# Performance work log

Hardware: AMD Instinct MI355X
Metric: run time of the kernel (lower is better)

## Reference

```python
import jax, jax.numpy as jnp
import numpy as np

B, T, IN, H, OUT = 256, 512, 128, 1024, 9  # batch, seq_len, input_size, hidden_dim, output_size(=9 coords)


def setup_inputs() -> dict:
    key = jax.random.key(0)
    ks = jax.random.split(key, 10)
    rn = lambda k, sh: jax.random.normal(k, sh, dtype=jnp.float32) * 0.05
    return {
        "x": rn(ks[0], (B, T, IN)),
        "W_ih": rn(ks[1], (4 * H, IN + OUT)),   # LSTMCell input weights (input_size + 9)
        "b_ih": rn(ks[2], (4 * H,)),
        "W_hh": rn(ks[3], (4 * H, H)),
        "b_hh": rn(ks[4], (4 * H,)),
        "W_h2h": rn(ks[5], (H, H)),
        "b_h2h": rn(ks[6], (H,)),
        "W_h2o": rn(ks[7], (OUT, H)),
        "b_h2o": rn(ks[8], (OUT,)),
        "lengths": jax.random.randint(ks[9], (B,), 1, T + 1).astype(jnp.int32),
    }


def reference(x, W_ih, b_ih, W_hh, b_hh, W_h2h, b_h2h, W_h2o, b_h2o, lengths):
    # Faithful to SimpleCharRNN.forward with use_corrector_flag=False (default):
    # per timestep: concat(x_t, prev_output) -> LSTMCell -> h2h -> h2o,
    # and NOTE the h2h output replaces h as the recurrent hidden state.
    batch = x.shape[0]
    hid = W_hh.shape[1]
    out_dim = W_h2o.shape[0]

    def step(carry, xt):
        h, c, out_prev = carry
        inp = jnp.concatenate([xt, out_prev], axis=-1)           # [B, IN+9]
        gates = inp @ W_ih.T + b_ih + h @ W_hh.T + b_hh          # [B, 4H]
        i, f, g, o = jnp.split(gates, 4, axis=-1)                # torch LSTMCell gate order
        i = jax.nn.sigmoid(i)
        f = jax.nn.sigmoid(f)
        g = jnp.tanh(g)
        o = jax.nn.sigmoid(o)
        c_new = f * c + i * g
        h_cell = o * jnp.tanh(c_new)
        h_new = h_cell @ W_h2h.T + b_h2h                         # h <- h2h(h)
        out_new = h_new @ W_h2o.T + b_h2o                        # output_i = h2o(h)
        return (h_new, c_new, out_new), out_new

    h0 = jnp.zeros((batch, hid), x.dtype)
    c0 = jnp.zeros((batch, hid), x.dtype)
    o0 = jnp.zeros((batch, out_dim), x.dtype)
    _, outs = jax.lax.scan(step, (h0, c0, o0), jnp.swapaxes(x, 0, 1))  # outs: [T, B, 9]
    answer = jnp.swapaxes(outs, 0, 1)                            # [B, T, 9]
    return answer, lengths
```

## Files before the change

kernel.cpp:

```cpp
#include <hip/hip_runtime.h>
#include <math.h>

#define TB 256
#define TT 512
#define TIN 128
#define TH 1024
#define TOUT 9
#define KD 1152

typedef _Float16 half8 __attribute__((ext_vector_type(8)));
typedef float f32x4 __attribute__((ext_vector_type(4)));

#define OB_WHF   0ull
#define SB_WHF   (128ull*2*36*64*8*2)
#define OB_WCB   (OB_WHF + SB_WHF)
#define SB_WCB   (9ull*1024*4)
#define OB_BCB   (OB_WCB + SB_WCB)
#define SB_BCB   64ull
#define OB_B0    (OB_BCB + SB_BCB)
#define SB_B0    (4096ull*4)
#define OB_BC    (OB_B0 + SB_B0)
#define SB_BC    (4096ull*4)
#define OB_H0    (OB_BC + SB_BC)
#define SB_H     (256ull*1024*2)
#define OB_H1    (OB_H0 + SB_H)
#define OB_GC    (OB_H1 + SB_H)
#define OB_END   (OB_GC + 8192ull)

__device__ __forceinline__ size_t frag_addr(int col, int k) {
  int q = col >> 10, hcol = col & 1023;
  int wcg = hcol >> 3, jj = hcol & 7;
  int c = (q << 3) | jj;
  int nt = c >> 4, n = c & 15;
  int kc = k >> 5, ls = (k >> 3) & 3, je = k & 7;
  return ((((size_t)wcg * 2 + nt) * 36 + kc) * 64 + ((ls << 4) | n)) * 8 + je;
}

__device__ __forceinline__ void st_h2_agent(_Float16* p, _Float16 v) {
  union { _Float16 h; unsigned short u; } c; c.h = v;
  __hip_atomic_store((unsigned short*)p, c.u, __ATOMIC_RELAXED, __HIP_MEMORY_SCOPE_AGENT);
}


__global__ __launch_bounds__(256) void k_combo(const float* __restrict__ W_h2o,
                                               const float* __restrict__ W_h2h,
                                               const float* __restrict__ b_h2h,
                                               const float* __restrict__ b_h2o,
                                               float* __restrict__ Wcombo,
                                               float* __restrict__ bcombo) {
  int gid = blockIdx.x * 256 + threadIdx.x;
  if (gid < 9 * 1024) {
    int r = gid >> 10, m = gid & 1023;
    float s = 0.f;
    for (int j = 0; j < 1024; ++j) s += W_h2o[r * 1024 + j] * W_h2h[j * 1024 + m];
    Wcombo[gid] = s;
  }
  if (gid < 9) {
    float s = b_h2o[gid];
    for (int j = 0; j < 1024; ++j) s += W_h2o[gid * 1024 + j] * b_h2h[j];
    bcombo[gid] = s;
  }
}

__global__ __launch_bounds__(256) void k_wblk(const float* __restrict__ W_hh,
                                              const float* __restrict__ W_ih,
                                              const float* __restrict__ W_h2o,
                                              const float* __restrict__ W_h2h,
                                              _Float16* __restrict__ Whf) {
  __shared__ float As2[16][68];
  __shared__ float Bs[16][68];
  __shared__ float Wio_s[64][12];
  __shared__ float Bo[9][16];
  const int tid = threadIdx.x;
  const int bm = (blockIdx.x & 15) * 64;
  const int bc = (blockIdx.x >> 4) * 64;
  const int tx = tid & 15, ty = tid >> 4;
  const int cl = tid >> 2, kq4 = tid & 3;

  for (int i = tid; i < 64 * 9; i += 256) {
    int row = i / 9, r = i % 9;
    Wio_s[row][r] = W_ih[(size_t)(bc + row) * 137 + 128 + r];
  }

  float acc[4][4];
#pragma unroll
  for (int i = 0; i < 4; ++i)
#pragma unroll
    for (int j = 0; j < 4; ++j) acc[i][j] = 0.f;

  for (int k0 = 0; k0 < 1024; k0 += 16) {
    __syncthreads();
    if (tid < 144) { int r = tid >> 4, kk = tid & 15; Bo[r][kk] = W_h2o[(size_t)r * 1024 + k0 + kk]; }
    { int kk = tid >> 4, q = tid & 15;
      float4 v = *(const float4*)(W_h2h + (size_t)(k0 + kk) * 1024 + bm + q * 4);
      *(float4*)&Bs[kk][q * 4] = v; }
    float4 av = *(const float4*)(W_hh + (size_t)(bc + cl) * 1024 + k0 + kq4 * 4);
    __syncthreads();
    {
      float c0 = 0.f, c1 = 0.f, c2 = 0.f, c3 = 0.f;
#pragma unroll
      for (int r = 0; r < 9; ++r) {
        float wio = Wio_s[cl][r];
        c0 += wio * Bo[r][kq4 * 4 + 0];
        c1 += wio * Bo[r][kq4 * 4 + 1];
        c2 += wio * Bo[r][kq4 * 4 + 2];
        c3 += wio * Bo[r][kq4 * 4 + 3];
      }
      As2[kq4 * 4 + 0][cl] = av.x + c0;
      As2[kq4 * 4 + 1][cl] = av.y + c1;
      As2[kq4 * 4 + 2][cl] = av.z + c2;
      As2[kq4 * 4 + 3][cl] = av.w + c3;
    }
    __syncthreads();
#pragma unroll
    for (int kk = 0; kk < 16; ++kk) {
      float4 a = *(const float4*)&As2[kk][ty * 4];
      float4 bv = *(const float4*)&Bs[kk][tx * 4];
      acc[0][0] += a.x * bv.x; acc[0][1] += a.x * bv.y; acc[0][2] += a.x * bv.z; acc[0][3] += a.x * bv.w;
      acc[1][0] += a.y * bv.x; acc[1][1] += a.y * bv.y; acc[1][2] += a.y * bv.z; acc[1][3] += a.y * bv.w;
      acc[2][0] += a.z * bv.x; acc[2][1] += a.z * bv.y; acc[2][2] += a.z * bv.z; acc[2][3] += a.z * bv.w;
      acc[3][0] += a.w * bv.x; acc[3][1] += a.w * bv.y; acc[3][2] += a.w * bv.z; acc[3][3] += a.w * bv.w;
    }
  }
#pragma unroll
  for (int i = 0; i < 4; ++i)
#pragma unroll
    for (int j = 0; j < 4; ++j) {
      int col = bc + ty * 4 + i;
      int m = bm + tx * 4 + j;
      Whf[frag_addr(col, 128 + m)] = (_Float16)acc[i][j];
    }
}

__global__ __launch_bounds__(256) void k_bias(const float* __restrict__ b_ih,
                                              const float* __restrict__ b_hh,
                                              const float* __restrict__ W_hh,
                                              const float* __restrict__ W_ih,
                                              const float* __restrict__ b_h2h,
                                              const float* __restrict__ bcombo,
                                              float* __restrict__ b0,
                                              float* __restrict__ bconst) {
  int col = blockIdx.x * 256 + threadIdx.x;
  float base = b_ih[col] + b_hh[col];
  b0[col] = base;
  float s = 0.f;
  for (int j = 0; j < 1024; ++j) s += W_hh[(size_t)col * 1024 + j] * b_h2h[j];
#pragma unroll
  for (int r = 0; r < 9; ++r) s += W_ih[(size_t)col * 137 + 128 + r] * bcombo[r];
  bconst[col] = base + s;
}

__global__ __launch_bounds__(256) void k_fillx(const float* __restrict__ W_ih,
                                               _Float16* __restrict__ Whf) {
  int gid = blockIdx.x * 256 + threadIdx.x;
  int col = gid >> 7, k = gid & 127;
  Whf[frag_addr(col, k)] = (_Float16)W_ih[(size_t)col * 137 + k];
}

__global__ void k_len(const int* __restrict__ len, float* __restrict__ dout) {
  int i = threadIdx.x;
  if (i < TB) dout[(size_t)TB * TT * TOUT + i] = (float)len[i];
}


__device__ __forceinline__ float sigm(float v) { return 1.f / (1.f + __expf(-v)); }
__device__ __forceinline__ float tanh_f(float v) {
  float e2 = __expf(2.f * v);
  return (e2 - 1.f) / (e2 + 1.f);
}

#define KEEP14(a) asm volatile("" :: "v"(a[0]), "v"(a[1]), "v"(a[2]), "v"(a[3]), \
  "v"(a[4]), "v"(a[5]), "v"(a[6]), "v"(a[7]), "v"(a[8]), "v"(a[9]), "v"(a[10]), \
  "v"(a[11]), "v"(a[12]), "v"(a[13]))
#define KEEP18(a) asm volatile("" :: "v"(a[0]), "v"(a[1]), "v"(a[2]), "v"(a[3]), \
  "v"(a[4]), "v"(a[5]), "v"(a[6]), "v"(a[7]), "v"(a[8]), "v"(a[9]), "v"(a[10]), \
  "v"(a[11]), "v"(a[12]), "v"(a[13]), "v"(a[14]), "v"(a[15]), "v"(a[16]), "v"(a[17]))

__global__ __launch_bounds__(512, 2) void k_main(const float* __restrict__ x,
                                                 const _Float16* __restrict__ Whf,
                                                 const float* __restrict__ Wc,
                                                 const float* __restrict__ b0,
                                                 const float* __restrict__ bcf,
                                                 const float* __restrict__ bcombo,
                                                 _Float16* __restrict__ hA,
                                                 _Float16* __restrict__ hB,
                                                 unsigned* __restrict__ gs,
                                                 float* __restrict__ dout) {
  __shared__ _Float16 Wl[2 * 36 * 64 * 8];
  __shared__ float gbuf[2][128][36];
  __shared__ float Wc_s[9][1024];
  __shared__ float bias_s[2][32];
  __shared__ float bco_s[12];
  __shared__ int sAbort;

  const int bx = blockIdx.x;
  const int half_id = bx >> 7;
  const int wcg = bx & 127;
  const int B0 = half_id * 128;
  const int myb = B0 + wcg;
  const int grp = wcg >> 4;
  const int tid = threadIdx.x;
  const int lane = tid & 63;
  const int wv = tid >> 6;
  const int mp = wv & 3, kh = wv >> 2;

  const size_t CH = (size_t)TB * 8;

  unsigned* hbase = gs + half_id * 1024;
  unsigned* gcnt_grp = hbase + grp * 32;
  unsigned* gcnt_root = hbase + 8 * 32;
  unsigned* gabort = gs + 1984;

  {
    const uint4* src = (const uint4*)(Whf + (size_t)wcg * (2 * 36 * 64 * 8));
    uint4* dst = (uint4*)Wl;
    for (int i = tid; i < 2 * 36 * 64 * 8 / 8; i += 512) dst[i] = src[i];
  }
  {
    const float4* src = (const float4*)Wc;
    float4* dst = (float4*)&Wc_s[0][0];
    for (int i = tid; i < 9 * 1024 / 4; i += 512) dst[i] = src[i];
  }
  if (tid == 0) sAbort = 0;
  if (tid < 9) bco_s[tid] = bcombo[tid];
  if (tid < 32) {
    int g = (tid >> 3) * 1024 + wcg * 8 + (tid & 7);
    bias_s[0][tid] = b0[g];
    bias_s[1][tid] = bcf[g];
  }
  float cs0 = 0.f, cs1 = 0.f;
  __syncthreads();

  const _Float16* ha = hA;
  _Float16* hn = hB;

  const int bA0 = B0 + mp * 32 + (lane & 15);
  const int bA1 = bA0 + 16;
  const int ko = (lane >> 4) * 8;
  const int chb = lane >> 4;
  const _Float16* wlb = Wl + (size_t)lane * 8 + (size_t)(kh * 18) * 512;
  unsigned myLead = 0;

  f32x4 acc00 = {0.f, 0.f, 0.f, 0.f};
  f32x4 acc01 = {0.f, 0.f, 0.f, 0.f};
  f32x4 acc10 = {0.f, 0.f, 0.f, 0.f};
  f32x4 acc11 = {0.f, 0.f, 0.f, 0.f};

#define XPART(tt) do { \
    const float* x0_ = x + ((size_t)bA0 * TT + (tt)) * TIN; \
    const float* x1_ = x + ((size_t)bA1 * TT + (tt)) * TIN; \
    _Pragma("unroll") \
    for (int i_ = 0; i_ < 4; ++i_) { \
      float4 p0 = *(const float4*)(x0_ + i_ * 32 + ko); \
      float4 p1 = *(const float4*)(x0_ + i_ * 32 + ko + 4); \
      float4 q0 = *(const float4*)(x1_ + i_ * 32 + ko); \
      float4 q1 = *(const float4*)(x1_ + i_ * 32 + ko + 4); \
      half8 v0_, v1_; \
      v0_[0] = (_Float16)p0.x; v0_[1] = (_Float16)p0.y; v0_[2] = (_Float16)p0.z; v0_[3] = (_Float16)p0.w; \
      v0_[4] = (_Float16)p1.x; v0_[5] = (_Float16)p1.y; v0_[6] = (_Float16)p1.z; v0_[7] = (_Float16)p1.w; \
      v1_[0] = (_Float16)q0.x; v1_[1] = (_Float16)q0.y; v1_[2] = (_Float16)q0.z; v1_[3] = (_Float16)q0.w; \
      v1_[4] = (_Float16)q1.x; v1_[5] = (_Float16)q1.y; v1_[6] = (_Float16)q1.z; v1_[7] = (_Float16)q1.w; \
      half8 bf0_ = *(const half8*)(wlb + (size_t)i_ * 512); \
      half8 bf1_ = *(const half8*)(wlb + (size_t)(36 + i_) * 512); \
      acc00 = __builtin_amdgcn_mfma_f32_16x16x32_f16(v0_, bf0_, acc00, 0, 0, 0); \
      acc01 = __builtin_amdgcn_mfma_f32_16x16x32_f16(v0_, bf1_, acc01, 0, 0, 0); \
      acc10 = __builtin_amdgcn_mfma_f32_16x16x32_f16(v1_, bf0_, acc10, 0, 0, 0); \
      acc11 = __builtin_amdgcn_mfma_f32_16x16x32_f16(v1_, bf1_, acc11, 0, 0, 0); \
    } \
  } while (0)

  if (kh == 0) XPART(0);

  for (int t = 0; t < TT; ++t) {
    const _Float16* hb0 = ha + (size_t)chb * CH + (size_t)bA0 * 8;
    const _Float16* hb1 = ha + (size_t)chb * CH + (size_t)bA1 * 8;
    if (kh == 0) {
      half8 a0[14], a1[14];
#pragma unroll
      for (int i = 0; i < 14; ++i) {
        a0[i] = *(const half8*)(hb0 + (size_t)(4 * (4 + i) - 16) * CH);
        a1[i] = *(const half8*)(hb1 + (size_t)(4 * (4 + i) - 16) * CH);
      }
      KEEP14(a0); KEEP14(a1);
      __builtin_amdgcn_sched_barrier(0);
#pragma unroll
      for (int i = 0; i < 14; ++i) {
        const int lc = 4 + i;
        half8 bf0 = *(const half8*)(wlb + (size_t)lc * 512);
        half8 bf1 = *(const half8*)(wlb + (size_t)(36 + lc) * 512);
        acc00 = __builtin_amdgcn_mfma_f32_16x16x32_f16(a0[i], bf0, acc00, 0, 0, 0);
        acc01 = __builtin_amdgcn_mfma_f32_16x16x32_f16(a0[i], bf1, acc01, 0, 0, 0);
        acc10 = __builtin_amdgcn_mfma_f32_16x16x32_f16(a1[i], bf0, acc10, 0, 0, 0);
        acc11 = __builtin_amdgcn_mfma_f32_16x16x32_f16(a1[i], bf1, acc11, 0, 0, 0);
      }
    } else {
      half8 a0[18], a1[18];
#pragma unroll
      for (int i = 0; i < 18; ++i) {
        a0[i] = *(const half8*)(hb0 + (size_t)(4 * i + 56) * CH);
        a1[i] = *(const half8*)(hb1 + (size_t)(4 * i + 56) * CH);
      }
      KEEP18(a0); KEEP18(a1);
      __builtin_amdgcn_sched_barrier(0);
#pragma unroll
      for (int i = 0; i < 18; ++i) {
        half8 bf0 = *(const half8*)(wlb + (size_t)i * 512);
        half8 bf1 = *(const half8*)(wlb + (size_t)(36 + i) * 512);
        acc00 = __builtin_amdgcn_mfma_f32_16x16x32_f16(a0[i], bf0, acc00, 0, 0, 0);
        acc01 = __builtin_amdgcn_mfma_f32_16x16x32_f16(a0[i], bf1, acc01, 0, 0, 0);
        acc10 = __builtin_amdgcn_mfma_f32_16x16x32_f16(a1[i], bf0, acc10, 0, 0, 0);
        acc11 = __builtin_amdgcn_mfma_f32_16x16x32_f16(a1[i], bf1, acc11, 0, 0, 0);
      }
    }
    {
      int rb0 = mp * 32 + (lane >> 4) * 4;
      int rb1 = rb0 + 16;
      int cc = lane & 15;
#pragma unroll
      for (int r = 0; r < 4; ++r) {
        gbuf[kh][rb0 + r][cc] = acc00[r];
        gbuf[kh][rb0 + r][16 + cc] = acc01[r];
        gbuf[kh][rb1 + r][cc] = acc10[r];
        gbuf[kh][rb1 + r][16 + cc] = acc11[r];
      }
    }
    __syncthreads();

    {
      const int fb = tid >> 3, fj = tid & 7;
      const float* bs = bias_s[(t > 0) ? 1 : 0];
      float vi = gbuf[0][fb][fj]      + gbuf[1][fb][fj]      + bs[fj];
      float vf = gbuf[0][fb][8 + fj]  + gbuf[1][fb][8 + fj]  + bs[8 + fj];
      float vg = gbuf[0][fb][16 + fj] + gbuf[1][fb][16 + fj] + bs[16 + fj];
      float vo = gbuf[0][fb][24 + fj] + gbuf[1][fb][24 + fj] + bs[24 + fj];
      float ig = sigm(vi), fg = sigm(vf), gg = tanh_f(vg), og = sigm(vo);
      float cn = fg * cs0 + ig * gg;
      cs0 = cn;
      st_h2_agent(hn + (size_t)wcg * CH + (size_t)(B0 + fb) * 8 + fj,
                  (_Float16)(og * tanh_f(cn)));

      const int fb2 = fb + 64;
      float vi2 = gbuf[0][fb2][fj]      + gbuf[1][fb2][fj]      + bs[fj];
      float vf2 = gbuf[0][fb2][8 + fj]  + gbuf[1][fb2][8 + fj]  + bs[8 + fj];
      float vg2 = gbuf[0][fb2][16 + fj] + gbuf[1][fb2][16 + fj] + bs[16 + fj];
      float vo2 = gbuf[0][fb2][24 + fj] + gbuf[1][fb2][24 + fj] + bs[24 + fj];
      float ig2 = sigm(vi2), fg2 = sigm(vf2), gg2 = tanh_f(vg2), og2 = sigm(vo2);
      float cn2 = fg2 * cs1 + ig2 * gg2;
      cs1 = cn2;
      st_h2_agent(hn + (size_t)wcg * CH + (size_t)(B0 + fb2) * 8 + fj,
                  (_Float16)(og2 * tanh_f(cn2)));
    }
    __threadfence_block();
    __syncthreads();

    if (tid == 0) {
      unsigned old = __hip_atomic_fetch_add(gcnt_grp, 1u, __ATOMIC_RELAXED, __HIP_MEMORY_SCOPE_AGENT);
      myLead = (old == (unsigned)(t + 1) * 16u - 1u);
      if (myLead)
        __hip_atomic_fetch_add(gcnt_root, 1u, __ATOMIC_RELAXED, __HIP_MEMORY_SCOPE_AGENT);
    }

    if (t > 0) {
      const _Float16* hxb = ha + (size_t)myb * 8;
      {
        float s = 0.f;
#pragma unroll
        for (int p = 0; p < 2; ++p) {
          int ch = 2 * lane + p;
          half8 hv = *(const half8*)(hxb + (size_t)ch * CH);
          const float* wr = &Wc_s[wv][ch * 8];
#pragma unroll
          for (int j = 0; j < 8; ++j) s += (float)hv[j] * wr[j];
        }
#pragma unroll
        for (int off = 32; off > 0; off >>= 1) s += __shfl_down(s, off, 64);
        if (lane == 0) dout[((size_t)myb * TT + (t - 1)) * TOUT + wv] = s + bco_s[wv];
      }
      if (wv == 0) {
        const float* wr8 = &Wc_s[8][0];
        float s = 0.f;
#pragma unroll
        for (int p = 0; p < 2; ++p) {
          int ch = 2 * lane + p;
          half8 hv = *(const half8*)(hxb + (size_t)ch * CH);
#pragma unroll
          for (int j = 0; j < 8; ++j) s += (float)hv[j] * wr8[ch * 8 + j];
        }
#pragma unroll
        for (int off = 32; off > 0; off >>= 1) s += __shfl_down(s, off, 64);
        if (lane == 0) dout[((size_t)myb * TT + (t - 1)) * TOUT + 8] = s + bco_s[8];
      }
    }

    acc00 = (f32x4){0.f, 0.f, 0.f, 0.f};
    acc01 = (f32x4){0.f, 0.f, 0.f, 0.f};
    acc10 = (f32x4){0.f, 0.f, 0.f, 0.f};
    acc11 = (f32x4){0.f, 0.f, 0.f, 0.f};
    if (kh == 0 && t + 1 < TT) XPART(t + 1);

    if (tid == 0) {
      bool ab = false;
      unsigned guard = 0;
      const unsigned tgt = (unsigned)(t + 1) * 8u;
      while (__hip_atomic_load(gcnt_root, __ATOMIC_RELAXED, __HIP_MEMORY_SCOPE_AGENT) < tgt) {
        __builtin_amdgcn_s_sleep(1);
        if (((++guard) & 255u) == 0u &&
            __hip_atomic_load(gabort, __ATOMIC_RELAXED, __HIP_MEMORY_SCOPE_AGENT) != 0u) { ab = true; break; }
        if (guard > 200000u) {
          __hip_atomic_store(gabort, 1u, __ATOMIC_RELAXED, __HIP_MEMORY_SCOPE_AGENT);
          ab = true; break;
        }
      }
      if (ab) {
        sAbort = 1;
      } else {
        (void)__hip_atomic_load(gcnt_root, __ATOMIC_ACQUIRE, __HIP_MEMORY_SCOPE_AGENT);
      }
    }
    __syncthreads();
    if (sAbort) return;

    const _Float16* tp = ha; ha = hn; hn = (_Float16*)tp;
  }

  {
    const _Float16* hxb = ha + (size_t)myb * 8;
    {
      float s = 0.f;
#pragma unroll
      for (int p = 0; p < 2; ++p) {
        int ch = 2 * lane + p;
        half8 hv = *(const half8*)(hxb + (size_t)ch * CH);
        const float* wr = &Wc_s[wv][ch * 8];
#pragma unroll
        for (int j = 0; j < 8; ++j) s += (float)hv[j] * wr[j];
      }
#pragma unroll
      for (int off = 32; off > 0; off >>= 1) s += __shfl_down(s, off, 64);
      if (lane == 0) dout[((size_t)myb * TT + (TT - 1)) * TOUT + wv] = s + bco_s[wv];
    }
    if (wv == 0) {
      const float* wr8 = &Wc_s[8][0];
      float s = 0.f;
#pragma unroll
      for (int p = 0; p < 2; ++p) {
        int ch = 2 * lane + p;
        half8 hv = *(const half8*)(hxb + (size_t)ch * CH);
#pragma unroll
        for (int j = 0; j < 8; ++j) s += (float)hv[j] * wr8[ch * 8 + j];
      }
#pragma unroll
      for (int off = 32; off > 0; off >>= 1) s += __shfl_down(s, off, 64);
      if (lane == 0) dout[((size_t)myb * TT + (TT - 1)) * TOUT + 8] = s + bco_s[8];
    }
  }
}


extern "C" void kernel_launch(void* const* d_in, const int* in_sizes, int n_in,
                              void* d_out, int out_size, void* d_ws, size_t ws_size,
                              hipStream_t stream) {
  if (ws_size < OB_END) return;

  const float* x     = (const float*)d_in[0];
  const float* W_ih  = (const float*)d_in[1];
  const float* b_ih  = (const float*)d_in[2];
  const float* W_hh  = (const float*)d_in[3];
  const float* b_hh  = (const float*)d_in[4];
  const float* W_h2h = (const float*)d_in[5];
  const float* b_h2h = (const float*)d_in[6];
  const float* W_h2o = (const float*)d_in[7];
  const float* b_h2o = (const float*)d_in[8];
  const int*   lens  = (const int*)d_in[9];

  char* ws = (char*)d_ws;
  float* dout    = (float*)d_out;
  _Float16* Whf  = (_Float16*)(ws + OB_WHF);
  float* Wcombo  = (float*)(ws + OB_WCB);
  float* bcombo  = (float*)(ws + OB_BCB);
  float* b0      = (float*)(ws + OB_B0);
  float* bconst  = (float*)(ws + OB_BC);
  _Float16* h0   = (_Float16*)(ws + OB_H0);
  _Float16* h1   = (_Float16*)(ws + OB_H1);
  unsigned* gs   = (unsigned*)(ws + OB_GC);

  hipMemsetAsync((void*)(ws + OB_H0), 0, OB_END - OB_H0, stream);

  k_combo<<<36, 256, 0, stream>>>(W_h2o, W_h2h, b_h2h, b_h2o, Wcombo, bcombo);
  k_wblk<<<1024, 256, 0, stream>>>(W_hh, W_ih, W_h2o, W_h2h, Whf);
  k_bias<<<16, 256, 0, stream>>>(b_ih, b_hh, W_hh, W_ih, b_h2h, bcombo, b0, bconst);
  k_fillx<<<2048, 256, 0, stream>>>(W_ih, Whf);
  k_len<<<1, 256, 0, stream>>>(lens, dout);

  k_main<<<256, 512, 0, stream>>>(x, Whf, Wcombo, b0, bconst, bcombo, h0, h1, gs, dout);
}
```

Measured before the change: 5.049 ms.

## Double block size to 1024 threads and split K reduction across four wave groups

```diff
diff --git a/kernel.cpp b/kernel.cpp
--- a/kernel.cpp
+++ b/kernel.cpp
@@ -169,25 +169,22 @@
   return (e2 - 1.f) / (e2 + 1.f);
 }
 
-#define KEEP14(a) asm volatile("" :: "v"(a[0]), "v"(a[1]), "v"(a[2]), "v"(a[3]), \
-  "v"(a[4]), "v"(a[5]), "v"(a[6]), "v"(a[7]), "v"(a[8]), "v"(a[9]), "v"(a[10]), \
-  "v"(a[11]), "v"(a[12]), "v"(a[13]))
-#define KEEP18(a) asm volatile("" :: "v"(a[0]), "v"(a[1]), "v"(a[2]), "v"(a[3]), \
-  "v"(a[4]), "v"(a[5]), "v"(a[6]), "v"(a[7]), "v"(a[8]), "v"(a[9]), "v"(a[10]), \
-  "v"(a[11]), "v"(a[12]), "v"(a[13]), "v"(a[14]), "v"(a[15]), "v"(a[16]), "v"(a[17]))
-
-__global__ __launch_bounds__(512, 2) void k_main(const float* __restrict__ x,
-                                                 const _Float16* __restrict__ Whf,
-                                                 const float* __restrict__ Wc,
-                                                 const float* __restrict__ b0,
-                                                 const float* __restrict__ bcf,
-                                                 const float* __restrict__ bcombo,
-                                                 _Float16* __restrict__ hA,
-                                                 _Float16* __restrict__ hB,
-                                                 unsigned* __restrict__ gs,
-                                                 float* __restrict__ dout) {
+#define KEEP5(a) asm volatile("" :: "v"(a[0]), "v"(a[1]), "v"(a[2]), "v"(a[3]), "v"(a[4]))
+#define KEEP9(a) asm volatile("" :: "v"(a[0]), "v"(a[1]), "v"(a[2]), "v"(a[3]), \
+  "v"(a[4]), "v"(a[5]), "v"(a[6]), "v"(a[7]), "v"(a[8]))
+
+__global__ __launch_bounds__(1024, 4) void k_main(const float* __restrict__ x,
+                                                  const _Float16* __restrict__ Whf,
+                                                  const float* __restrict__ Wc,
+                                                  const float* __restrict__ b0,
+                                                  const float* __restrict__ bcf,
+                                                  const float* __restrict__ bcombo,
+                                                  _Float16* __restrict__ hA,
+                                                  _Float16* __restrict__ hB,
+                                                  unsigned* __restrict__ gs,
+                                                  float* __restrict__ dout) {
   __shared__ _Float16 Wl[2 * 36 * 64 * 8];
-  __shared__ float gbuf[2][128][36];
+  __shared__ _Float16 gbuf[4][128][36];
   __shared__ float Wc_s[9][1024];
   __shared__ float bias_s[2][32];
   __shared__ float bco_s[12];
@@ -202,7 +199,7 @@
   const int tid = threadIdx.x;
   const int lane = tid & 63;
   const int wv = tid >> 6;
-  const int mp = wv & 3, kh = wv >> 2;
+  const int mp = wv & 3, kq = wv >> 2;
 
   const size_t CH = (size_t)TB * 8;
 
@@ -214,12 +211,12 @@
   {
     const uint4* src = (const uint4*)(Whf + (size_t)wcg * (2 * 36 * 64 * 8));
     uint4* dst = (uint4*)Wl;
-    for (int i = tid; i < 2 * 36 * 64 * 8 / 8; i += 512) dst[i] = src[i];
+    for (int i = tid; i < 2 * 36 * 64 * 8 / 8; i += 1024) dst[i] = src[i];
   }
   {
     const float4* src = (const float4*)Wc;
     float4* dst = (float4*)&Wc_s[0][0];
-    for (int i = tid; i < 9 * 1024 / 4; i += 512) dst[i] = src[i];
+    for (int i = tid; i < 9 * 1024 / 4; i += 1024) dst[i] = src[i];
   }
   if (tid == 0) sAbort = 0;
   if (tid < 9) bco_s[tid] = bcombo[tid];
@@ -228,7 +225,7 @@
     bias_s[0][tid] = b0[g];
     bias_s[1][tid] = bcf[g];
   }
-  float cs0 = 0.f, cs1 = 0.f;
+  float cs = 0.f;
   __syncthreads();
 
   const _Float16* ha = hA;
@@ -238,7 +235,7 @@
   const int bA1 = bA0 + 16;
   const int ko = (lane >> 4) * 8;
   const int chb = lane >> 4;
-  const _Float16* wlb = Wl + (size_t)lane * 8 + (size_t)(kh * 18) * 512;
+  const _Float16* wlb = Wl + (size_t)lane * 8;
   unsigned myLead = 0;
 
   f32x4 acc00 = {0.f, 0.f, 0.f, 0.f};
@@ -269,43 +266,44 @@
     } \
   } while (0)
 
-  if (kh == 0) XPART(0);
+  if (kq == 0) XPART(0);
 
   for (int t = 0; t < TT; ++t) {
     const _Float16* hb0 = ha + (size_t)chb * CH + (size_t)bA0 * 8;
     const _Float16* hb1 = ha + (size_t)chb * CH + (size_t)bA1 * 8;
-    if (kh == 0) {
-      half8 a0[14], a1[14];
-#pragma unroll
-      for (int i = 0; i < 14; ++i) {
-        a0[i] = *(const half8*)(hb0 + (size_t)(4 * (4 + i) - 16) * CH);
-        a1[i] = *(const half8*)(hb1 + (size_t)(4 * (4 + i) - 16) * CH);
-      }
-      KEEP14(a0); KEEP14(a1);
+    if (kq == 0) {
+      half8 a0[5], a1[5];
+#pragma unroll
+      for (int i = 0; i < 5; ++i) {
+        a0[i] = *(const half8*)(hb0 + (size_t)(4 * i) * CH);
+        a1[i] = *(const half8*)(hb1 + (size_t)(4 * i) * CH);
+      }
+      KEEP5(a0); KEEP5(a1);
       __builtin_amdgcn_sched_barrier(0);
 #pragma unroll
-      for (int i = 0; i < 14; ++i) {
-        const int lc = 4 + i;
-        half8 bf0 = *(const half8*)(wlb + (size_t)lc * 512);
-        half8 bf1 = *(const half8*)(wlb + (size_t)(36 + lc) * 512);
+      for (int i = 0; i < 5; ++i) {
+        const int kcg = 4 + i;
+        half8 bf0 = *(const half8*)(wlb + (size_t)kcg * 512);
+        half8 bf1 = *(const half8*)(wlb + (size_t)(36 + kcg) * 512);
         acc00 = __builtin_amdgcn_mfma_f32_16x16x32_f16(a0[i], bf0, acc00, 0, 0, 0);
         acc01 = __builtin_amdgcn_mfma_f32_16x16x32_f16(a0[i], bf1, acc01, 0, 0, 0);
         acc10 = __builtin_amdgcn_mfma_f32_16x16x32_f16(a1[i], bf0, acc10, 0, 0, 0);
         acc11 = __builtin_amdgcn_mfma_f32_16x16x32_f16(a1[i], bf1, acc11, 0, 0, 0);
       }
     } else {
-      half8 a0[18], a1[18];
-#pragma unroll
-      for (int i = 0; i < 18; ++i) {
-        a0[i] = *(const half8*)(hb0 + (size_t)(4 * i + 56) * CH);
-        a1[i] = *(const half8*)(hb1 + (size_t)(4 * i + 56) * CH);
-      }
-      KEEP18(a0); KEEP18(a1);
+      half8 a0[9], a1[9];
+#pragma unroll
+      for (int i = 0; i < 9; ++i) {
+        a0[i] = *(const half8*)(hb0 + (size_t)(4 * (9 * kq + i) - 16) * CH);
+        a1[i] = *(const half8*)(hb1 + (size_t)(4 * (9 * kq + i) - 16) * CH);
+      }
+      KEEP9(a0); KEEP9(a1);
       __builtin_amdgcn_sched_barrier(0);
 #pragma unroll
-      for (int i = 0; i < 18; ++i) {
-        half8 bf0 = *(const half8*)(wlb + (size_t)i * 512);
-        half8 bf1 = *(const half8*)(wlb + (size_t)(36 + i) * 512);
+      for (int i = 0; i < 9; ++i) {
+        const int kcg = 9 * kq + i;
+        half8 bf0 = *(const half8*)(wlb + (size_t)kcg * 512);
+        half8 bf1 = *(const half8*)(wlb + (size_t)(36 + kcg) * 512);
         acc00 = __builtin_amdgcn_mfma_f32_16x16x32_f16(a0[i], bf0, acc00, 0, 0, 0);
         acc01 = __builtin_amdgcn_mfma_f32_16x16x32_f16(a0[i], bf1, acc01, 0, 0, 0);
         acc10 = __builtin_amdgcn_mfma_f32_16x16x32_f16(a1[i], bf0, acc10, 0, 0, 0);
@@ -318,10 +316,10 @@
       int cc = lane & 15;
 #pragma unroll
       for (int r = 0; r < 4; ++r) {
-        gbuf[kh][rb0 + r][cc] = acc00[r];
-        gbuf[kh][rb0 + r][16 + cc] = acc01[r];
-        gbuf[kh][rb1 + r][cc] = acc10[r];
-        gbuf[kh][rb1 + r][16 + cc] = acc11[r];
+        gbuf[kq][rb0 + r][cc] = (_Float16)acc00[r];
+        gbuf[kq][rb0 + r][16 + cc] = (_Float16)acc01[r];
+        gbuf[kq][rb1 + r][cc] = (_Float16)acc10[r];
+        gbuf[kq][rb1 + r][16 + cc] = (_Float16)acc11[r];
       }
     }
     __syncthreads();
@@ -329,26 +327,19 @@
     {
       const int fb = tid >> 3, fj = tid & 7;
       const float* bs = bias_s[(t > 0) ? 1 : 0];
-      float vi = gbuf[0][fb][fj]      + gbuf[1][fb][fj]      + bs[fj];
-      float vf = gbuf[0][fb][8 + fj]  + gbuf[1][fb][8 + fj]  + bs[8 + fj];
-      float vg = gbuf[0][fb][16 + fj] + gbuf[1][fb][16 + fj] + bs[16 + fj];
-      float vo = gbuf[0][fb][24 + fj] + gbuf[1][fb][24 + fj] + bs[24 + fj];
+      float vi = (float)gbuf[0][fb][fj]      + (float)gbuf[1][fb][fj]
+               + (float)gbuf[2][fb][fj]      + (float)gbuf[3][fb][fj]      + bs[fj];
+      float vf = (float)gbuf[0][fb][8 + fj]  + (float)gbuf[1][fb][8 + fj]
+               + (float)gbuf[2][fb][8 + fj]  + (float)gbuf[3][fb][8 + fj]  + bs[8 + fj];
+      float vg = (float)gbuf[0][fb][16 + fj] + (float)gbuf[1][fb][16 + fj]
+               + (float)gbuf[2][fb][16 + fj] + (float)gbuf[3][fb][16 + fj] + bs[16 + fj];
+      float vo = (float)gbuf[0][fb][24 + fj] + (float)gbuf[1][fb][24 + fj]
+               + (float)gbuf[2][fb][24 + fj] + (float)gbuf[3][fb][24 + fj] + bs[24 + fj];
       float ig = sigm(vi), fg = sigm(vf), gg = tanh_f(vg), og = sigm(vo);
-      float cn = fg * cs0 + ig * gg;
-      cs0 = cn;
+      float cn = fg * cs + ig * gg;
+      cs = cn;
       st_h2_agent(hn + (size_t)wcg * CH + (size_t)(B0 + fb) * 8 + fj,
                   (_Float16)(og * tanh_f(cn)));
-
-      const int fb2 = fb + 64;
-      float vi2 = gbuf[0][fb2][fj]      + gbuf[1][fb2][fj]      + bs[fj];
-      float vf2 = gbuf[0][fb2][8 + fj]  + gbuf[1][fb2][8 + fj]  + bs[8 + fj];
-      float vg2 = gbuf[0][fb2][16 + fj] + gbuf[1][fb2][16 + fj] + bs[16 + fj];
-      float vo2 = gbuf[0][fb2][24 + fj] + gbuf[1][fb2][24 + fj] + bs[24 + fj];
-      float ig2 = sigm(vi2), fg2 = sigm(vf2), gg2 = tanh_f(vg2), og2 = sigm(vo2);
-      float cn2 = fg2 * cs1 + ig2 * gg2;
-      cs1 = cn2;
-      st_h2_agent(hn + (size_t)wcg * CH + (size_t)(B0 + fb2) * 8 + fj,
-                  (_Float16)(og2 * tanh_f(cn2)));
     }
     __threadfence_block();
     __syncthreads();
@@ -360,43 +351,27 @@
         __hip_atomic_fetch_add(gcnt_root, 1u, __ATOMIC_RELAXED, __HIP_MEMORY_SCOPE_AGENT);
     }
 
-    if (t > 0) {
+    if (t > 0 && wv < 9) {
       const _Float16* hxb = ha + (size_t)myb * 8;
-      {
-        float s = 0.f;
-#pragma unroll
-        for (int p = 0; p < 2; ++p) {
-          int ch = 2 * lane + p;
-          half8 hv = *(const half8*)(hxb + (size_t)ch * CH);
-          const float* wr = &Wc_s[wv][ch * 8];
-#pragma unroll
-          for (int j = 0; j < 8; ++j) s += (float)hv[j] * wr[j];
-        }
-#pragma unroll
-        for (int off = 32; off > 0; off >>= 1) s += __shfl_down(s, off, 64);
-        if (lane == 0) dout[((size_t)myb * TT + (t - 1)) * TOUT + wv] = s + bco_s[wv];
-      }
-      if (wv == 0) {
-        const float* wr8 = &Wc_s[8][0];
-        float s = 0.f;
-#pragma unroll
-        for (int p = 0; p < 2; ++p) {
-          int ch = 2 * lane + p;
-          half8 hv = *(const half8*)(hxb + (size_t)ch * CH);
-#pragma unroll
-          for (int j = 0; j < 8; ++j) s += (float)hv[j] * wr8[ch * 8 + j];
-        }
-#pragma unroll
-        for (int off = 32; off > 0; off >>= 1) s += __shfl_down(s, off, 64);
-        if (lane == 0) dout[((size_t)myb * TT + (t - 1)) * TOUT + 8] = s + bco_s[8];
-      }
+      float s = 0.f;
+#pragma unroll
+      for (int p = 0; p < 2; ++p) {
+        int ch = 2 * lane + p;
+        half8 hv = *(const half8*)(hxb + (size_t)ch * CH);
+        const float* wr = &Wc_s[wv][ch * 8];
+#pragma unroll
+        for (int j = 0; j < 8; ++j) s += (float)hv[j] * wr[j];
+      }
+#pragma unroll
+      for (int off = 32; off > 0; off >>= 1) s += __shfl_down(s, off, 64);
+      if (lane == 0) dout[((size_t)myb * TT + (t - 1)) * TOUT + wv] = s + bco_s[wv];
     }
 
     acc00 = (f32x4){0.f, 0.f, 0.f, 0.f};
     acc01 = (f32x4){0.f, 0.f, 0.f, 0.f};
     acc10 = (f32x4){0.f, 0.f, 0.f, 0.f};
     acc11 = (f32x4){0.f, 0.f, 0.f, 0.f};
-    if (kh == 0 && t + 1 < TT) XPART(t + 1);
+    if (kq == 0 && t + 1 < TT) XPART(t + 1);
 
     if (tid == 0) {
       bool ab = false;
@@ -423,36 +398,20 @@
     const _Float16* tp = ha; ha = hn; hn = (_Float16*)tp;
   }
 
-  {
+  if (wv < 9) {
     const _Float16* hxb = ha + (size_t)myb * 8;
-    {
-      float s = 0.f;
-#pragma unroll
-      for (int p = 0; p < 2; ++p) {
-        int ch = 2 * lane + p;
-        half8 hv = *(const half8*)(hxb + (size_t)ch * CH);
-        const float* wr = &Wc_s[wv][ch * 8];
-#pragma unroll
-        for (int j = 0; j < 8; ++j) s += (float)hv[j] * wr[j];
-      }
-#pragma unroll
-      for (int off = 32; off > 0; off >>= 1) s += __shfl_down(s, off, 64);
-      if (lane == 0) dout[((size_t)myb * TT + (TT - 1)) * TOUT + wv] = s + bco_s[wv];
-    }
-    if (wv == 0) {
-      const float* wr8 = &Wc_s[8][0];
-      float s = 0.f;
-#pragma unroll
-      for (int p = 0; p < 2; ++p) {
-        int ch = 2 * lane + p;
-        half8 hv = *(const half8*)(hxb + (size_t)ch * CH);
-#pragma unroll
-        for (int j = 0; j < 8; ++j) s += (float)hv[j] * wr8[ch * 8 + j];
-      }
-#pragma unroll
-      for (int off = 32; off > 0; off >>= 1) s += __shfl_down(s, off, 64);
-      if (lane == 0) dout[((size_t)myb * TT + (TT - 1)) * TOUT + 8] = s + bco_s[8];
-    }
+    float s = 0.f;
+#pragma unroll
+    for (int p = 0; p < 2; ++p) {
+      int ch = 2 * lane + p;
+      half8 hv = *(const half8*)(hxb + (size_t)ch * CH);
+      const float* wr = &Wc_s[wv][ch * 8];
+#pragma unroll
+      for (int j = 0; j < 8; ++j) s += (float)hv[j] * wr[j];
+    }
+#pragma unroll
+    for (int off = 32; off > 0; off >>= 1) s += __shfl_down(s, off, 64);
+    if (lane == 0) dout[((size_t)myb * TT + (TT - 1)) * TOUT + wv] = s + bco_s[wv];
   }
 }
 
@@ -492,5 +451,5 @@
   k_fillx<<<2048, 256, 0, stream>>>(W_ih, Whf);
   k_len<<<1, 256, 0, stream>>>(lens, dout);
 
-  k_main<<<256, 512, 0, stream>>>(x, Whf, Wcombo, b0, bconst, bcombo, h0, h1, gs, dout);
-}
+  k_main<<<256, 1024, 0, stream>>>(x, Whf, Wcombo, b0, bconst, bcombo, h0, h1, gs, dout);
+}
```

After: 6.236 ms. +23.5%, slower.

## Retile recurrent LSTM kernel to 64-batch quarters with 16 hidden columns per block

Applied to the files above, without the earlier changes.

```diff
diff --git a/kernel.cpp b/kernel.cpp
--- a/kernel.cpp
+++ b/kernel.cpp
@@ -12,7 +12,7 @@
 typedef float f32x4 __attribute__((ext_vector_type(4)));
 
 #define OB_WHF   0ull
-#define SB_WHF   (128ull*2*36*64*8*2)
+#define SB_WHF   (64ull*4*36*64*8*2)
 #define OB_WCB   (OB_WHF + SB_WHF)
 #define SB_WCB   (9ull*1024*4)
 #define OB_BCB   (OB_WCB + SB_WCB)
@@ -29,11 +29,9 @@
 
 __device__ __forceinline__ size_t frag_addr(int col, int k) {
   int q = col >> 10, hcol = col & 1023;
-  int wcg = hcol >> 3, jj = hcol & 7;
-  int c = (q << 3) | jj;
-  int nt = c >> 4, n = c & 15;
+  int wcg2 = hcol >> 4, jj = hcol & 15;
   int kc = k >> 5, ls = (k >> 3) & 3, je = k & 7;
-  return ((((size_t)wcg * 2 + nt) * 36 + kc) * 64 + ((ls << 4) | n)) * 8 + je;
+  return ((((size_t)wcg2 * 4 + q) * 36 + kc) * 64 + ((ls << 4) | jj)) * 8 + je;
 }
 
 __device__ __forceinline__ void st_h2_agent(_Float16* p, _Float16 v) {
@@ -186,48 +184,45 @@
                                                  _Float16* __restrict__ hB,
                                                  unsigned* __restrict__ gs,
                                                  float* __restrict__ dout) {
-  __shared__ _Float16 Wl[2 * 36 * 64 * 8];
-  __shared__ float gbuf[2][128][36];
-  __shared__ float Wc_s[9][1024];
-  __shared__ float bias_s[2][32];
-  __shared__ float bco_s[12];
+  __shared__ _Float16 Wl[4 * 36 * 64 * 8];
+  __shared__ _Float16 gbuf[64][72];
   __shared__ int sAbort;
 
   const int bx = blockIdx.x;
-  const int half_id = bx >> 7;
-  const int wcg = bx & 127;
-  const int B0 = half_id * 128;
-  const int myb = B0 + wcg;
-  const int grp = wcg >> 4;
+  const int qd = bx >> 6;
+  const int wcg2 = bx & 63;
+  const int B0 = qd * 64;
+  const int myb = B0 + wcg2;
+  const int grp = wcg2 >> 3;
   const int tid = threadIdx.x;
   const int lane = tid & 63;
   const int wv = tid >> 6;
-  const int mp = wv & 3, kh = wv >> 2;
+  const int mp = wv & 1, np = (wv >> 1) & 1, kh = wv >> 2;
 
   const size_t CH = (size_t)TB * 8;
 
-  unsigned* hbase = gs + half_id * 1024;
-  unsigned* gcnt_grp = hbase + grp * 32;
-  unsigned* gcnt_root = hbase + 8 * 32;
-  unsigned* gabort = gs + 1984;
+  unsigned* qbase = gs + qd * 512;
+  unsigned* gcnt_grp = qbase + grp * 32;
+  unsigned* gcnt_root = qbase + 8 * 32;
+  unsigned* gabort = gs + 500;
 
   {
-    const uint4* src = (const uint4*)(Whf + (size_t)wcg * (2 * 36 * 64 * 8));
+    const uint4* src = (const uint4*)(Whf + (size_t)wcg2 * (4 * 36 * 64 * 8));
     uint4* dst = (uint4*)Wl;
-    for (int i = tid; i < 2 * 36 * 64 * 8 / 8; i += 512) dst[i] = src[i];
-  }
-  {
-    const float4* src = (const float4*)Wc;
-    float4* dst = (float4*)&Wc_s[0][0];
-    for (int i = tid; i < 9 * 1024 / 4; i += 512) dst[i] = src[i];
+    for (int i = tid; i < 4 * 36 * 64 * 8 / 8; i += 512) dst[i] = src[i];
   }
   if (tid == 0) sAbort = 0;
-  if (tid < 9) bco_s[tid] = bcombo[tid];
-  if (tid < 32) {
-    int g = (tid >> 3) * 1024 + wcg * 8 + (tid & 7);
-    bias_s[0][tid] = b0[g];
-    bias_s[1][tid] = bcf[g];
-  }
+
+  const int fb_i = tid >> 3, fj_i = tid & 7;
+  const int cb = wcg2 * 16;
+  float bC0 = bcf[cb + fj_i],          bC1 = bcf[1024 + cb + fj_i];
+  float bC2 = bcf[2048 + cb + fj_i],   bC3 = bcf[3072 + cb + fj_i];
+  float bC4 = bcf[cb + 8 + fj_i],      bC5 = bcf[1024 + cb + 8 + fj_i];
+  float bC6 = bcf[2048 + cb + 8 + fj_i], bC7 = bcf[3072 + cb + 8 + fj_i];
+  float bZ0 = b0[cb + fj_i],           bZ1 = b0[1024 + cb + fj_i];
+  float bZ2 = b0[2048 + cb + fj_i],    bZ3 = b0[3072 + cb + fj_i];
+  float bZ4 = b0[cb + 8 + fj_i],       bZ5 = b0[1024 + cb + 8 + fj_i];
+  float bZ6 = b0[2048 + cb + 8 + fj_i], bZ7 = b0[3072 + cb + 8 + fj_i];
   float cs0 = 0.f, cs1 = 0.f;
   __syncthreads();
 
@@ -238,7 +233,8 @@
   const int bA1 = bA0 + 16;
   const int ko = (lane >> 4) * 8;
   const int chb = lane >> 4;
-  const _Float16* wlb = Wl + (size_t)lane * 8 + (size_t)(kh * 18) * 512;
+  const _Float16* wlb0 = Wl + (size_t)(2 * np) * 18432 + (size_t)lane * 8;
+  const _Float16* wlb1 = wlb0 + 18432;
   unsigned myLead = 0;
 
   f32x4 acc00 = {0.f, 0.f, 0.f, 0.f};
@@ -260,8 +256,8 @@
       v0_[4] = (_Float16)p1.x; v0_[5] = (_Float16)p1.y; v0_[6] = (_Float16)p1.z; v0_[7] = (_Float16)p1.w; \
       v1_[0] = (_Float16)q0.x; v1_[1] = (_Float16)q0.y; v1_[2] = (_Float16)q0.z; v1_[3] = (_Float16)q0.w; \
       v1_[4] = (_Float16)q1.x; v1_[5] = (_Float16)q1.y; v1_[6] = (_Float16)q1.z; v1_[7] = (_Float16)q1.w; \
-      half8 bf0_ = *(const half8*)(wlb + (size_t)i_ * 512); \
-      half8 bf1_ = *(const half8*)(wlb + (size_t)(36 + i_) * 512); \
+      half8 bf0_ = *(const half8*)(wlb0 + (size_t)i_ * 512); \
+      half8 bf1_ = *(const half8*)(wlb1 + (size_t)i_ * 512); \
       acc00 = __builtin_amdgcn_mfma_f32_16x16x32_f16(v0_, bf0_, acc00, 0, 0, 0); \
       acc01 = __builtin_amdgcn_mfma_f32_16x16x32_f16(v0_, bf1_, acc01, 0, 0, 0); \
       acc10 = __builtin_amdgcn_mfma_f32_16x16x32_f16(v1_, bf0_, acc10, 0, 0, 0); \
@@ -278,16 +274,16 @@
       half8 a0[14], a1[14];
 #pragma unroll
       for (int i = 0; i < 14; ++i) {
-        a0[i] = *(const half8*)(hb0 + (size_t)(4 * (4 + i) - 16) * CH);
-        a1[i] = *(const half8*)(hb1 + (size_t)(4 * (4 + i) - 16) * CH);
+        a0[i] = *(const half8*)(hb0 + (size_t)(4 * i) * CH);
+        a1[i] = *(const half8*)(hb1 + (size_t)(4 * i) * CH);
       }
       KEEP14(a0); KEEP14(a1);
       __builtin_amdgcn_sched_barrier(0);
 #pragma unroll
       for (int i = 0; i < 14; ++i) {
-        const int lc = 4 + i;
-        half8 bf0 = *(const half8*)(wlb + (size_t)lc * 512);
-        half8 bf1 = *(const half8*)(wlb + (size_t)(36 + lc) * 512);
+        const int kcg = 4 + i;
+        half8 bf0 = *(const half8*)(wlb0 + (size_t)kcg * 512);
+        half8 bf1 = *(const half8*)(wlb1 + (size_t)kcg * 512);
         acc00 = __builtin_amdgcn_mfma_f32_16x16x32_f16(a0[i], bf0, acc00, 0, 0, 0);
         acc01 = __builtin_amdgcn_mfma_f32_16x16x32_f16(a0[i], bf1, acc01, 0, 0, 0);
         acc10 = __builtin_amdgcn_mfma_f32_16x16x32_f16(a1[i], bf0, acc10, 0, 0, 0);
@@ -304,8 +300,9 @@
       __builtin_amdgcn_sched_barrier(0);
 #pragma unroll
       for (int i = 0; i < 18; ++i) {
-        half8 bf0 = *(const half8*)(wlb + (size_t)i * 512);
-        half8 bf1 = *(const half8*)(wlb + (size_t)(36 + i) * 512);
+        const int kcg = 18 + i;
+        half8 bf0 = *(const half8*)(wlb0 + (size_t)kcg * 512);
+        half8 bf1 = *(const half8*)(wlb1 + (size_t)kcg * 512);
         acc00 = __builtin_amdgcn_mfma_f32_16x16x32_f16(a0[i], bf0, acc00, 0, 0, 0);
         acc01 = __builtin_amdgcn_mfma_f32_16x16x32_f16(a0[i], bf1, acc01, 0, 0, 0);
         acc10 = __builtin_amdgcn_mfma_f32_16x16x32_f16(a1[i], bf0, acc10, 0, 0, 0);
@@ -315,39 +312,53 @@
     {
       int rb0 = mp * 32 + (lane >> 4) * 4;
       int rb1 = rb0 + 16;
-      int cc = lane & 15;
-#pragma unroll
-      for (int r = 0; r < 4; ++r) {
-        gbuf[kh][rb0 + r][cc] = acc00[r];
-        gbuf[kh][rb0 + r][16 + cc] = acc01[r];
-        gbuf[kh][rb1 + r][cc] = acc10[r];
-        gbuf[kh][rb1 + r][16 + cc] = acc11[r];
-      }
-    }
-    __syncthreads();
+      int cc0 = np * 32 + (lane & 15);
+      int cc1 = cc0 + 16;
+      if (kh == 0) {
+#pragma unroll
+        for (int r = 0; r < 4; ++r) {
+          gbuf[rb0 + r][cc0] = (_Float16)acc00[r];
+          gbuf[rb0 + r][cc1] = (_Float16)acc01[r];
+          gbuf[rb1 + r][cc0] = (_Float16)acc10[r];
+          gbuf[rb1 + r][cc1] = (_Float16)acc11[r];
+        }
+      }
+      __syncthreads();
+      if (kh == 1) {
+#pragma unroll
+        for (int r = 0; r < 4; ++r) {
+          gbuf[rb0 + r][cc0] = (_Float16)((float)gbuf[rb0 + r][cc0] + acc00[r]);
+          gbuf[rb0 + r][cc1] = (_Float16)((float)gbuf[rb0 + r][cc1] + acc01[r]);
+          gbuf[rb1 + r][cc0] = (_Float16)((float)gbuf[rb1 + r][cc0] + acc10[r]);
+          gbuf[rb1 + r][cc1] = (_Float16)((float)gbuf[rb1 + r][cc1] + acc11[r]);
+        }
+      }
+      __syncthreads();
+    }
 
     {
-      const int fb = tid >> 3, fj = tid & 7;
-      const float* bs = bias_s[(t > 0) ? 1 : 0];
-      float vi = gbuf[0][fb][fj]      + gbuf[1][fb][fj]      + bs[fj];
-      float vf = gbuf[0][fb][8 + fj]  + gbuf[1][fb][8 + fj]  + bs[8 + fj];
-      float vg = gbuf[0][fb][16 + fj] + gbuf[1][fb][16 + fj] + bs[16 + fj];
-      float vo = gbuf[0][fb][24 + fj] + gbuf[1][fb][24 + fj] + bs[24 + fj];
+      const bool later = (t > 0);
+      float b_0 = later ? bC0 : bZ0, b_1 = later ? bC1 : bZ1;
+      float b_2 = later ? bC2 : bZ2, b_3 = later ? bC3 : bZ3;
+      float b_4 = later ? bC4 : bZ4, b_5 = later ? bC5 : bZ5;
+      float b_6 = later ? bC6 : bZ6, b_7 = later ? bC7 : bZ7;
+      float vi = (float)gbuf[fb_i][fj_i]      + b_0;
+      float vf = (float)gbuf[fb_i][16 + fj_i] + b_1;
+      float vg = (float)gbuf[fb_i][32 + fj_i] + b_2;
+      float vo = (float)gbuf[fb_i][48 + fj_i] + b_3;
       float ig = sigm(vi), fg = sigm(vf), gg = tanh_f(vg), og = sigm(vo);
       float cn = fg * cs0 + ig * gg;
       cs0 = cn;
-      st_h2_agent(hn + (size_t)wcg * CH + (size_t)(B0 + fb) * 8 + fj,
+      st_h2_agent(hn + (size_t)(2 * wcg2) * CH + (size_t)(B0 + fb_i) * 8 + fj_i,
                   (_Float16)(og * tanh_f(cn)));
-
-      const int fb2 = fb + 64;
-      float vi2 = gbuf[0][fb2][fj]      + gbuf[1][fb2][fj]      + bs[fj];
-      float vf2 = gbuf[0][fb2][8 + fj]  + gbuf[1][fb2][8 + fj]  + bs[8 + fj];
-      float vg2 = gbuf[0][fb2][16 + fj] + gbuf[1][fb2][16 + fj] + bs[16 + fj];
-      float vo2 = gbuf[0][fb2][24 + fj] + gbuf[1][fb2][24 + fj] + bs[24 + fj];
+      float vi2 = (float)gbuf[fb_i][8 + fj_i]  + b_4;
+      float vf2 = (float)gbuf[fb_i][24 + fj_i] + b_5;
+      float vg2 = (float)gbuf[fb_i][40 + fj_i] + b_6;
+      float vo2 = (float)gbuf[fb_i][56 + fj_i] + b_7;
       float ig2 = sigm(vi2), fg2 = sigm(vf2), gg2 = tanh_f(vg2), og2 = sigm(vo2);
       float cn2 = fg2 * cs1 + ig2 * gg2;
       cs1 = cn2;
-      st_h2_agent(hn + (size_t)wcg * CH + (size_t)(B0 + fb2) * 8 + fj,
+      st_h2_agent(hn + (size_t)(2 * wcg2 + 1) * CH + (size_t)(B0 + fb_i) * 8 + fj_i,
                   (_Float16)(og2 * tanh_f(cn2)));
     }
     __threadfence_block();
@@ -355,7 +366,7 @@
 
     if (tid == 0) {
       unsigned old = __hip_atomic_fetch_add(gcnt_grp, 1u, __ATOMIC_RELAXED, __HIP_MEMORY_SCOPE_AGENT);
-      myLead = (old == (unsigned)(t + 1) * 16u - 1u);
+      myLead = (old == (unsigned)(t + 1) * 8u - 1u);
       if (myLead)
         __hip_atomic_fetch_add(gcnt_root, 1u, __ATOMIC_RELAXED, __HIP_MEMORY_SCOPE_AGENT);
     }
@@ -363,32 +374,36 @@
     if (t > 0) {
       const _Float16* hxb = ha + (size_t)myb * 8;
       {
+        const float* wcp = Wc + (size_t)wv * 1024;
         float s = 0.f;
 #pragma unroll
         for (int p = 0; p < 2; ++p) {
           int ch = 2 * lane + p;
           half8 hv = *(const half8*)(hxb + (size_t)ch * CH);
-          const float* wr = &Wc_s[wv][ch * 8];
-#pragma unroll
-          for (int j = 0; j < 8; ++j) s += (float)hv[j] * wr[j];
+          float4 wa = *(const float4*)(wcp + ch * 8);
+          float4 wb = *(const float4*)(wcp + ch * 8 + 4);
+          s += (float)hv[0] * wa.x + (float)hv[1] * wa.y + (float)hv[2] * wa.z + (float)hv[3] * wa.w
+             + (float)hv[4] * wb.x + (float)hv[5] * wb.y + (float)hv[6] * wb.z + (float)hv[7] * wb.w;
         }
 #pragma unroll
         for (int off = 32; off > 0; off >>= 1) s += __shfl_down(s, off, 64);
-        if (lane == 0) dout[((size_t)myb * TT + (t - 1)) * TOUT + wv] = s + bco_s[wv];
+        if (lane == 0) dout[((size_t)myb * TT + (t - 1)) * TOUT + wv] = s + bcombo[wv];
       }
       if (wv == 0) {
-        const float* wr8 = &Wc_s[8][0];
+        const float* wcp = Wc + 8 * 1024;
         float s = 0.f;
 #pragma unroll
         for (int p = 0; p < 2; ++p) {
           int ch = 2 * lane + p;
           half8 hv = *(const half8*)(hxb + (size_t)ch * CH);
-#pragma unroll
-          for (int j = 0; j < 8; ++j) s += (float)hv[j] * wr8[ch * 8 + j];
+          float4 wa = *(const float4*)(wcp + ch * 8);
+          float4 wb = *(const float4*)(wcp + ch * 8 + 4);
+          s += (float)hv[0] * wa.x + (float)hv[1] * wa.y + (float)hv[2] * wa.z + (float)hv[3] * wa.w
+             + (float)hv[4] * wb.x + (float)hv[5] * wb.y + (float)hv[6] * wb.z + (float)hv[7] * wb.w;
         }
 #pragma unroll
         for (int off = 32; off > 0; off >>= 1) s += __shfl_down(s, off, 64);
-        if (lane == 0) dout[((size_t)myb * TT + (t - 1)) * TOUT + 8] = s + bco_s[8];
+        if (lane == 0) dout[((size_t)myb * TT + (t - 1)) * TOUT + 8] = s + bcombo[8];
       }
     }
 
@@ -426,32 +441,36 @@
   {
     const _Float16* hxb = ha + (size_t)myb * 8;
     {
+      const float* wcp = Wc + (size_t)wv * 1024;
       float s = 0.f;
 #pragma unroll
       for (int p = 0; p < 2; ++p) {
         int ch = 2 * lane + p;
         half8 hv = *(const half8*)(hxb + (size_t)ch * CH);
-        const float* wr = &Wc_s[wv][ch * 8];
-#pragma unroll
-        for (int j = 0; j < 8; ++j) s += (float)hv[j] * wr[j];
+        float4 wa = *(const float4*)(wcp + ch * 8);
+        float4 wb = *(const float4*)(wcp + ch * 8 + 4);
+        s += (float)hv[0] * wa.x + (float)hv[1] * wa.y + (float)hv[2] * wa.z + (float)hv[3] * wa.w
+           + (float)hv[4] * wb.x + (float)hv[5] * wb.y + (float)hv[6] * wb.z + (float)hv[7] * wb.w;
       }
 #pragma unroll
       for (int off = 32; off > 0; off >>= 1) s += __shfl_down(s, off, 64);
-      if (lane == 0) dout[((size_t)myb * TT + (TT - 1)) * TOUT + wv] = s + bco_s[wv];
+      if (lane == 0) dout[((size_t)myb * TT + (TT - 1)) * TOUT + wv] = s + bcombo[wv];
     }
     if (wv == 0) {
-      const float* wr8 = &Wc_s[8][0];
+      const float* wcp = Wc + 8 * 1024;
       float s = 0.f;
 #pragma unroll
       for (int p = 0; p < 2; ++p) {
         int ch = 2 * lane + p;
         half8 hv = *(const half8*)(hxb + (size_t)ch * CH);
-#pragma unroll
-        for (int j = 0; j < 8; ++j) s += (float)hv[j] * wr8[ch * 8 + j];
+        float4 wa = *(const float4*)(wcp + ch * 8);
+        float4 wb = *(const float4*)(wcp + ch * 8 + 4);
+        s += (float)hv[0] * wa.x + (float)hv[1] * wa.y + (float)hv[2] * wa.z + (float)hv[3] * wa.w
+           + (float)hv[4] * wb.x + (float)hv[5] * wb.y + (float)hv[6] * wb.z + (float)hv[7] * wb.w;
       }
 #pragma unroll
       for (int off = 32; off > 0; off >>= 1) s += __shfl_down(s, off, 64);
-      if (lane == 0) dout[((size_t)myb * TT + (TT - 1)) * TOUT + 8] = s + bco_s[8];
+      if (lane == 0) dout[((size_t)myb * TT + (TT - 1)) * TOUT + 8] = s + bcombo[8];
     }
   }
 }
```

Result: no change. 5.033 ms (-0.3%).
